# Kernel optimization log

Measured on AMD Instinct MI355X. Metric: run time of the kernel, lower is better.

The kernel has to match this reference:

```python
import jax, jax.numpy as jnp
import numpy as np

L, B, T, I, H, O = 2, 64, 256, 512, 1024, 256
HIDDEN_WEIGHT = 0.5  # placement_weight = 1 - hidden_weight
# dropout is identity in eval mode (reference is deterministic)


def setup_inputs() -> dict:
    key = jax.random.key(0)
    ks = jax.random.split(key, 20)
    def unif(k, shape, fan):
        b = 1.0 / np.sqrt(fan)
        return jax.random.uniform(k, shape, jnp.float32, -b, b)
    lengths = jax.random.randint(ks[4], (B,), 0, T + 1)
    lengths = lengths.at[0].set(T).at[1].set(0)  # exercise full-length and zero-length paths
    return {
        "step_input": jax.random.normal(ks[0], (B, T, I), jnp.float32),
        "clstm_hidden": jax.random.normal(ks[1], (B, H), jnp.float32),
        "hidden": jax.random.normal(ks[2], (L, B, H), jnp.float32),
        "cell": jax.random.normal(ks[3], (L, B, H), jnp.float32),
        "input_lengths": lengths.astype(jnp.int64),
        # LSTM params, PyTorch gate order [i, f, g, o]
        "w_ih0": unif(ks[5], (4 * H, I), H), "w_hh0": unif(ks[6], (4 * H, H), H),
        "b_ih0": unif(ks[7], (4 * H,), H), "b_hh0": unif(ks[8], (4 * H,), H),
        "w_ih1": unif(ks[9], (4 * H, H), H), "w_hh1": unif(ks[10], (4 * H, H), H),
        "b_ih1": unif(ks[11], (4 * H,), H), "b_hh1": unif(ks[12], (4 * H,), H),
        "w1": unif(ks[13], (H, H), H), "b1": unif(ks[14], (H,), H),
        "w2": unif(ks[15], (O, H), H), "b2": unif(ks[16], (O,), H),
    }


def compute_weighted_hidden(clstm_hidden, hidden, lens):
    # vectorized version of the per-(layer,batch) min-max rescale loop
    cmin = jnp.min(clstm_hidden, axis=-1, keepdims=True)            # [B,1]
    crange = jnp.max(clstm_hidden, axis=-1, keepdims=True) - cmin   # [B,1]
    safe_cr = jnp.where(crange > 0, crange, 1.0)
    s = jnp.where(crange > 0, (clstm_hidden - cmin) / safe_cr, clstm_hidden)  # [B,H]
    hmin = jnp.min(hidden, axis=-1, keepdims=True)                  # [L,B,1]
    hrange = jnp.max(hidden, axis=-1, keepdims=True) - hmin         # [L,B,1]
    s2 = jnp.where(hrange > 0, hmin + s[None] * hrange,
                   jnp.broadcast_to(s[None], hidden.shape))         # [L,B,H]
    c = jnp.where((lens == 0)[None, :, None], clstm_hidden[None], s2)
    return HIDDEN_WEIGHT * hidden + (1.0 - HIDDEN_WEIGHT) * c


def lstm_forward(x, h0, c0, lens, layer_params):
    # x: [B,T,I]; h0,c0: [L,B,H]; lens already clamped to >=1
    t_idx = jnp.arange(x.shape[1])

    def step(carry, xt_t):
        h, c = carry                      # each [L,B,H]
        xt, t = xt_t                      # xt: [B,I]
        valid = (t < lens)[:, None]       # [B,1]
        inp = xt
        hs, cs = [], []
        for l, (wih, whh, bih, bhh) in enumerate(layer_params):
            gates = inp @ wih.T + bih + h[l] @ whh.T + bhh   # [B,4H]
            i, f, g, o = jnp.split(gates, 4, axis=-1)
            i, f, o = jax.nn.sigmoid(i), jax.nn.sigmoid(f), jax.nn.sigmoid(o)
            g = jnp.tanh(g)
            c_new = f * c[l] + i * g
            h_new = o * jnp.tanh(c_new)
            hs.append(jnp.where(valid, h_new, h[l]))
            cs.append(jnp.where(valid, c_new, c[l]))
            inp = jnp.where(valid, h_new, 0.0)
        out_t = inp                        # top layer output, zeroed on padding
        return (jnp.stack(hs), jnp.stack(cs)), out_t

    (hn, cn), outs = jax.lax.scan(step, (h0, c0), (x.transpose(1, 0, 2), t_idx))
    return outs.transpose(1, 0, 2), hn, cn  # [B,T,H], [L,B,H], [L,B,H]


def reference(step_input, clstm_hidden, hidden, cell, input_lengths,
              w_ih0, w_hh0, b_ih0, b_hh0, w_ih1, w_hh1, b_ih1, b_hh1,
              w1, b1, w2, b2):
    weighted_hidden = compute_weighted_hidden(clstm_hidden, hidden, input_lengths)
    lens = jnp.clip(input_lengths, 1, None)  # torch.clamp(min=1)
    layer_params = [(w_ih0, w_hh0, b_ih0, b_hh0), (w_ih1, w_hh1, b_ih1, b_hh1)]
    lstm_out, hn, cn = lstm_forward(step_input, weighted_hidden, cell, lens, layer_params)
    # dropout layers are identity in eval mode
    h1 = jax.nn.relu(lstm_out @ w1.T + b1)
    logits = jax.nn.relu(h1 @ w2.T + b2)  # [B,T,O]
    zero = (input_lengths == 0)
    logits = jnp.where(zero[:, None, None], 0.0, logits)
    hn = jnp.where(zero[None, :, None], 0.0, hn)
    cn = jnp.where(zero[None, :, None], 0.0, cn)
    return logits, hn, cn
```

## Files before the change

### kernel.cpp

```cpp
#include <hip/hip_runtime.h>


typedef __bf16 bf16x8 __attribute__((ext_vector_type(8)));
typedef float f32x4 __attribute__((ext_vector_type(4)));
typedef int i32x4 __attribute__((ext_vector_type(4)));

__device__ __forceinline__ unsigned short f2bf(float f) {
  unsigned u = __float_as_uint(f);
  u = u + 0x7FFFu + ((u >> 16) & 1u);
  return (unsigned short)(u >> 16);
}
__device__ __forceinline__ float sigm_(float x) { return 1.f / (1.f + __expf(-x)); }
__device__ __forceinline__ float tanh_(float x) { return 1.f - 2.f / (__expf(2.f * x) + 1.f); }

__device__ __forceinline__ int hxoff(int b, int u) {
  return (b >> 4) * 16384 + (u >> 5) * 512 + ((u >> 3) & 3) * 128 + (b & 15) * 8 + (u & 7);
}

__global__ void cvt_kernel(const float* __restrict__ s, unsigned short* __restrict__ d, int n) {
  int i = (blockIdx.x * 256 + threadIdx.x) * 4;
  if (i < n) {
    float4 v = *reinterpret_cast<const float4*>(s + i);
    ushort4 o = make_ushort4(f2bf(v.x), f2bf(v.y), f2bf(v.z), f2bf(v.w));
    *reinterpret_cast<ushort4*>(d + i) = o;
  }
}

__global__ __launch_bounds__(256) void prep_kernel(
    const float* __restrict__ clstm, const float* __restrict__ hidden,
    const float* __restrict__ cell, const int* __restrict__ lens,
    float* __restrict__ hstate, float* __restrict__ cstate,
    unsigned short* __restrict__ h0buf, unsigned short* __restrict__ h1buf,
    const float* __restrict__ bih0, const float* __restrict__ bhh0,
    const float* __restrict__ bih1, const float* __restrict__ bhh1,
    float* __restrict__ bias0, float* __restrict__ bias1p,
    unsigned* __restrict__ bar) {
  const int tid = threadIdx.x, blk = blockIdx.x;
  const int l = blk >> 6, b = blk & 63;
  const float* crow = clstm + b * 1024;
  const float* hrow = hidden + ((size_t)l * 64 + b) * 1024;
  float cmn = 3.4e38f, cmx = -3.4e38f, hmn = 3.4e38f, hmx = -3.4e38f;
  for (int i = tid; i < 1024; i += 256) {
    float c = crow[i], h = hrow[i];
    cmn = fminf(cmn, c); cmx = fmaxf(cmx, c);
    hmn = fminf(hmn, h); hmx = fmaxf(hmx, h);
  }
#pragma unroll
  for (int off = 32; off > 0; off >>= 1) {
    cmn = fminf(cmn, __shfl_xor(cmn, off));
    cmx = fmaxf(cmx, __shfl_xor(cmx, off));
    hmn = fminf(hmn, __shfl_xor(hmn, off));
    hmx = fmaxf(hmx, __shfl_xor(hmx, off));
  }
  __shared__ float red[4][4];
  int wv = tid >> 6;
  if ((tid & 63) == 0) { red[wv][0] = cmn; red[wv][1] = cmx; red[wv][2] = hmn; red[wv][3] = hmx; }
  __syncthreads();
  cmn = fminf(fminf(red[0][0], red[1][0]), fminf(red[2][0], red[3][0]));
  cmx = fmaxf(fmaxf(red[0][1], red[1][1]), fmaxf(red[2][1], red[3][1]));
  hmn = fminf(fminf(red[0][2], red[1][2]), fminf(red[2][2], red[3][2]));
  hmx = fmaxf(fmaxf(red[0][3], red[1][3]), fmaxf(red[2][3], red[3][3]));
  const float crange = cmx - cmn, hrange = hmx - hmn;
  const int len = lens[b];
  const size_t base = ((size_t)l * 64 + b) * 1024;
  unsigned short* dst = (l == 0) ? h0buf : (h1buf + 65536);
  for (int i = tid; i < 1024; i += 256) {
    float cv = crow[i], hv = hrow[i];
    float s = (crange > 0.f) ? (cv - cmn) / crange : cv;
    float s2 = (hrange > 0.f) ? (hmn + s * hrange) : s;
    float cc = (len == 0) ? cv : s2;
    float w = 0.5f * hv + 0.5f * cc;
    hstate[base + i] = w;
    cstate[base + i] = cell[base + i];
    dst[hxoff(b, i)] = f2bf(w);
  }
  if (blk == 0) {
    for (int n = tid; n < 4096; n += 256) {
      bias0[n] = bih0[n] + bhh0[n];
      bias1p[(n & 1023) * 4 + (n >> 10)] = bih1[n] + bhh1[n];
    }
    for (int n = tid; n < 32768; n += 256) bar[n] = 0u;
  }
}

template <int AMODE, int EPI>
__global__ __launch_bounds__(256) void gemm_kernel(
    const void* __restrict__ Ap, const unsigned short* __restrict__ Bw,
    void* __restrict__ Cout, const float* __restrict__ bias,
    const int* __restrict__ lens, int M, int N, int K, int t0) {
  __shared__ unsigned short Al[128][40];
  __shared__ unsigned short Bl[128][40];
  const int tid = threadIdx.x;
  const int m0 = blockIdx.y * 128, n0 = blockIdx.x * 128;
  const int srow = tid >> 2;
  const int c8 = (tid & 3) * 8;
  size_t aoff0, aoff1;
  {
    int r = m0 + srow, r2 = r + 64;
    if (AMODE == 0) {
      aoff0 = (size_t)r * K; aoff1 = (size_t)r2 * K;
    } else {
      aoff0 = ((size_t)(r & 63) * 256 + t0 + (r >> 6)) * K;
      aoff1 = ((size_t)(r2 & 63) * 256 + t0 + (r2 >> 6)) * K;
    }
  }
  const size_t boff0 = (size_t)(n0 + srow) * K, boff1 = (size_t)(n0 + srow + 64) * K;
  const int wave = tid >> 6, lane = tid & 63, ln = lane & 15, quad = lane >> 4;
  const int mq = (wave >> 1) * 64, nq = (wave & 1) * 64;
  f32x4 acc[4][4] = {};
  const int nkt = K >> 5;
  for (int kt = 0; kt < nkt; ++kt) {
    const int kc = kt * 32 + c8;
    if (AMODE == 1) {
      const float* A = (const float*)Ap;
      const float* p0 = A + aoff0 + kc;
      const float* p1 = A + aoff1 + kc;
      float4 v0 = *reinterpret_cast<const float4*>(p0);
      float4 v0b = *reinterpret_cast<const float4*>(p0 + 4);
      float4 v1 = *reinterpret_cast<const float4*>(p1);
      float4 v1b = *reinterpret_cast<const float4*>(p1 + 4);
      *reinterpret_cast<ushort4*>(&Al[srow][c8]) =
          make_ushort4(f2bf(v0.x), f2bf(v0.y), f2bf(v0.z), f2bf(v0.w));
      *reinterpret_cast<ushort4*>(&Al[srow][c8 + 4]) =
          make_ushort4(f2bf(v0b.x), f2bf(v0b.y), f2bf(v0b.z), f2bf(v0b.w));
      *reinterpret_cast<ushort4*>(&Al[srow + 64][c8]) =
          make_ushort4(f2bf(v1.x), f2bf(v1.y), f2bf(v1.z), f2bf(v1.w));
      *reinterpret_cast<ushort4*>(&Al[srow + 64][c8 + 4]) =
          make_ushort4(f2bf(v1b.x), f2bf(v1b.y), f2bf(v1b.z), f2bf(v1b.w));
    } else {
      const unsigned short* A = (const unsigned short*)Ap;
      *reinterpret_cast<int4*>(&Al[srow][c8]) = *reinterpret_cast<const int4*>(A + aoff0 + kc);
      *reinterpret_cast<int4*>(&Al[srow + 64][c8]) = *reinterpret_cast<const int4*>(A + aoff1 + kc);
    }
    *reinterpret_cast<int4*>(&Bl[srow][c8]) = *reinterpret_cast<const int4*>(Bw + boff0 + kc);
    *reinterpret_cast<int4*>(&Bl[srow + 64][c8]) = *reinterpret_cast<const int4*>(Bw + boff1 + kc);
    __syncthreads();
    bf16x8 af[4], bfr[4];
#pragma unroll
    for (int i = 0; i < 4; ++i) {
      af[i] = *reinterpret_cast<const bf16x8*>(&Al[mq + i * 16 + ln][quad * 8]);
      bfr[i] = *reinterpret_cast<const bf16x8*>(&Bl[nq + i * 16 + ln][quad * 8]);
    }
#pragma unroll
    for (int i = 0; i < 4; ++i)
#pragma unroll
      for (int j = 0; j < 4; ++j)
        acc[i][j] = __builtin_amdgcn_mfma_f32_16x16x32_bf16(af[i], bfr[j], acc[i][j], 0, 0, 0);
    __syncthreads();
  }
#pragma unroll
  for (int i = 0; i < 4; ++i) {
    int mmb = m0 + mq + i * 16 + quad * 4;
#pragma unroll
    for (int j = 0; j < 4; ++j) {
      int nn = n0 + nq + j * 16 + ln;
      float bv = bias[nn];
#pragma unroll
      for (int r = 0; r < 4; ++r) {
        int mm = mmb + r;
        float v = acc[i][j][r] + bv;
        if (EPI >= 1) v = fmaxf(v, 0.f);
        if (EPI == 2) {
          if (lens[mm >> 8] == 0) v = 0.f;
          ((float*)Cout)[(size_t)mm * N + nn] = v;
        } else if (EPI == 1) {
          ((unsigned short*)Cout)[(size_t)mm * N + nn] = f2bf(v);
        } else {
          size_t idx = ((size_t)mm * 128 + ((nn >> 3) & 127)) * 32 + (nn & 7) * 4 + (nn >> 10);
          ((float*)Cout)[idx] = v;
        }
      }
    }
  }
}

#define HLo(dst, ptr, off) \
  asm volatile("global_load_dwordx4 %0, %1, off offset:" off " sc0 sc1" \
               : "=v"(dst) : "v"(ptr))
#define HL4(h0, h1, h2, h3, ptr) \
  HLo(h0, ptr, "0"); HLo(h1, ptr, "1024"); HLo(h2, ptr, "2048"); HLo(h3, ptr, "3072")
#define HLF(dst, ptr) \
  asm volatile("global_load_dwordx4 %0, %1, off sc0 sc1" : "=v"(dst) : "v"(ptr))
#define HST(ptr, val) \
  asm volatile("global_store_dwordx4 %0, %1, off sc0 sc1" :: "v"(ptr), "v"(val) : "memory")

__global__ __launch_bounds__(512) void rec2_kernel(
    const unsigned short* __restrict__ whh0b,
    const unsigned short* __restrict__ wih1b,
    const unsigned short* __restrict__ whh1b,
    const float* __restrict__ G2,
    const float* __restrict__ bias1p,
    unsigned short* __restrict__ h0buf,
    unsigned short* __restrict__ h1buf,
    float* __restrict__ pre1buf,
    float* __restrict__ hstate, float* __restrict__ cstate,
    unsigned short* __restrict__ h1out,
    const int* __restrict__ lens, int t0, int nint, unsigned* __restrict__ bar) {
  __shared__ unsigned short wlds[32 * 1032];
  __shared__ float glds[2][64][73];
  __shared__ unsigned short hsh[64][16];
  const int tid = threadIdx.x;
  const int bid = blockIdx.x;
  const bool isL1 = bid >= 128;
  const int g = bid & 127;
  {
    int r = tid >> 4;
    int c0 = (tid & 15) * 64;
    const unsigned short* src;
    if (!isL1)
      src = wih1b + (size_t)((r >> 3) * 1024 + g * 8 + (r & 7)) * 1024;
    else
      src = whh1b + (size_t)((2 + (r >> 4)) * 1024 + g * 16 + (r & 15)) * 1024;
    const i32x4* s4 = reinterpret_cast<const i32x4*>(src + c0);
    i32x4* dst = reinterpret_cast<i32x4*>(wlds + r * 1032 + c0);
#pragma unroll
    for (int j = 0; j < 8; ++j) dst[j] = s4[j];
  }
  const int wave = tid >> 6, lane = tid & 63, ln = lane & 15, quad = lane >> 4;
  const int mt = wave & 3, kw = wave >> 2;
  bf16x8 bregA[16], bregB[16];
  {
    const unsigned short *bpA, *bpB;
    if (!isL1) {
      bpA = whh0b + (size_t)((ln >> 3) * 1024 + g * 8 + (ln & 7)) * 1024 + kw * 512 + quad * 8;
      bpB = whh0b + (size_t)((2 + (ln >> 3)) * 1024 + g * 8 + (ln & 7)) * 1024 + kw * 512 + quad * 8;
    } else {
      bpA = whh1b + (size_t)(g * 16 + ln) * 1024 + kw * 512 + quad * 8;
      bpB = whh1b + (size_t)(1024 + g * 16 + ln) * 1024 + kw * 512 + quad * 8;
    }
#pragma unroll
    for (int kt = 0; kt < 16; ++kt) {
      bregA[kt] = *reinterpret_cast<const bf16x8*>(bpA + kt * 32);
      bregB[kt] = *reinterpret_cast<const bf16x8*>(bpB + kt * 32);
    }
  }
  const int b = tid >> 3, ul = tid & 7;
  const size_t sb0 = (size_t)(isL1 ? 65536 : 0) + (size_t)b * 1024 +
                     (isL1 ? g * 16 + ul : g * 8 + ul);
  float cm0 = cstate[sb0], hm0 = hstate[sb0];
  float cm1 = 0.f, hm1 = 0.f;
  if (isL1) { cm1 = cstate[sb0 + 8]; hm1 = hstate[sb0 + 8]; }
  int lv0 = lens[b];
  const int len = lv0 < 1 ? 1 : lv0;
  int lvA = lens[mt * 16 + ln];
  const int lenmA = lvA < 1 ? 1 : lvA;
  f32x4 b1a = {0.f, 0.f, 0.f, 0.f}, b1b = {0.f, 0.f, 0.f, 0.f};
  if (isL1) {
    b1a = *reinterpret_cast<const f32x4*>(bias1p + (g * 16 + ul) * 4);
    b1b = *reinterpret_cast<const f32x4*>(bias1p + (g * 16 + 8 + ul) * 4);
  }
  int lenp = 257;
  if (isL1 && tid < 128) { int lv = lens[tid >> 1]; lenp = lv < 1 ? 1 : lv; }
  const int puboff = (tid >> 4) * 16384 + (g >> 2) * 512 + (g & 3) * 128 + (tid & 15) * 8;
  const int pub1off = ((tid >> 1) >> 4) * 16384 + (g >> 1) * 512 +
                      ((g * 2 + (tid & 1)) & 3) * 128 + ((tid >> 1) & 15) * 8;
  const bf16x8 z8 = {};
  const i32x4 zi = {};
  __syncthreads();

  for (int k = 0; k < nint; ++k) {
    const int s = t0 + k;
    const bool actG = (!isL1) && (k < 64);
    const bool actP = (!isL1) && (s >= 1) && (s <= 256);
    const bool actL = isL1 && (s >= 2);
    if (actG || actP || actL) {
      f32x4 pga = {0.f, 0.f, 0.f, 0.f}, pgb = {0.f, 0.f, 0.f, 0.f};
      if (isL1) {
        const float* pr = pre1buf + (size_t)((s - 2) & 3) * 262144 +
                          ((size_t)b * 1024 + g * 16) * 4;
        HLF(pga, pr + ul * 4);
        HLF(pgb, pr + (8 + ul) * 4);
      }
      bf16x8 hf[16];
      const unsigned short* p = (isL1 ? h1buf + ((s - 1) & 1) * 65536
                                      : h0buf + (s & 1) * 65536) +
                                mt * 16384 + kw * 8192 + lane * 8;
      HL4(hf[0], hf[1], hf[2], hf[3], p);
      HL4(hf[4], hf[5], hf[6], hf[7], p + 2048);
      HL4(hf[8], hf[9], hf[10], hf[11], p + 4096);
      HL4(hf[12], hf[13], hf[14], hf[15], p + 6144);
      if (actG)
        pga = *reinterpret_cast<const f32x4*>(
            G2 + (((size_t)(k * 64 + b)) * 128 + g) * 32 + ul * 4);
      const bool maskA = (!isL1) && ((s - 1) >= lenmA);
      f32x4 acc0 = {0.f, 0.f, 0.f, 0.f}, acc1 = acc0, acc2 = acc0, acc3 = acc0;
      const unsigned short* wp = wlds + ln * 1032 + kw * 512 + quad * 8;
      asm volatile("s_waitcnt vmcnt(8)" ::: "memory");
      __builtin_amdgcn_sched_barrier(0);
#pragma unroll
      for (int kt = 0; kt < 8; ++kt) {
        const unsigned short* c = wp + kt * 32;
        bf16x8 bC = *reinterpret_cast<const bf16x8*>(c);
        bf16x8 bD = *reinterpret_cast<const bf16x8*>(c + 16512);
        bf16x8 a_ = hf[kt];
        acc0 = __builtin_amdgcn_mfma_f32_16x16x32_bf16(a_, bregA[kt], acc0, 0, 0, 0);
        acc1 = __builtin_amdgcn_mfma_f32_16x16x32_bf16(a_, bregB[kt], acc1, 0, 0, 0);
        bf16x8 am = maskA ? z8 : a_;
        acc2 = __builtin_amdgcn_mfma_f32_16x16x32_bf16(am, bC, acc2, 0, 0, 0);
        acc3 = __builtin_amdgcn_mfma_f32_16x16x32_bf16(am, bD, acc3, 0, 0, 0);
      }
      asm volatile("s_waitcnt vmcnt(0)" ::: "memory");
      __builtin_amdgcn_sched_barrier(0);
#pragma unroll
      for (int kt = 8; kt < 16; ++kt) {
        const unsigned short* c = wp + kt * 32;
        bf16x8 bC = *reinterpret_cast<const bf16x8*>(c);
        bf16x8 bD = *reinterpret_cast<const bf16x8*>(c + 16512);
        bf16x8 a_ = hf[kt];
        acc0 = __builtin_amdgcn_mfma_f32_16x16x32_bf16(a_, bregA[kt], acc0, 0, 0, 0);
        acc1 = __builtin_amdgcn_mfma_f32_16x16x32_bf16(a_, bregB[kt], acc1, 0, 0, 0);
        bf16x8 am = maskA ? z8 : a_;
        acc2 = __builtin_amdgcn_mfma_f32_16x16x32_bf16(am, bC, acc2, 0, 0, 0);
        acc3 = __builtin_amdgcn_mfma_f32_16x16x32_bf16(am, bD, acc3, 0, 0, 0);
      }
#pragma unroll
      for (int r = 0; r < 4; ++r) {
        float* gp = &glds[kw][mt * 16 + quad * 4 + r][0];
        gp[ln] = acc0[r]; gp[16 + ln] = acc1[r];
        gp[32 + ln] = acc2[r]; gp[48 + ln] = acc3[r];
      }
      __syncthreads();
      const float* g0 = &glds[0][b][0];
      const float* g1 = &glds[1][b][0];
      if (actG) {
        float pi = g0[ul] + g1[ul] + pga.x;
        float pf = g0[8 + ul] + g1[8 + ul] + pga.y;
        float pgg = g0[16 + ul] + g1[16 + ul] + pga.z;
        float po = g0[24 + ul] + g1[24 + ul] + pga.w;
        float ig = sigm_(pi), fg = sigm_(pf), gv = tanh_(pgg), og = sigm_(po);
        float cn_ = fg * cm0 + ig * gv;
        float hn_ = og * tanh_(cn_);
        if (s < len) { cm0 = cn_; hm0 = hn_; }
        hsh[b][ul] = f2bf(hm0);
      }
      if (actP) {
        f32x4 pv;
        pv.x = g0[32 + ul] + g1[32 + ul];
        pv.y = g0[40 + ul] + g1[40 + ul];
        pv.z = g0[48 + ul] + g1[48 + ul];
        pv.w = g0[56 + ul] + g1[56 + ul];
        float* pd = pre1buf + (size_t)((s - 1) & 3) * 262144 +
                    (size_t)b * 4096 + g * 32 + ul * 4;
        HST(pd, pv);
      }
      if (actL) {
        {
          float pi = g0[ul] + g1[ul] + pga.x + b1a.x;
          float pf = g0[16 + ul] + g1[16 + ul] + pga.y + b1a.y;
          float pgg = g0[32 + ul] + g1[32 + ul] + pga.z + b1a.z;
          float po = g0[48 + ul] + g1[48 + ul] + pga.w + b1a.w;
          float ig = sigm_(pi), fg = sigm_(pf), gv = tanh_(pgg), og = sigm_(po);
          float cn_ = fg * cm0 + ig * gv;
          float hn_ = og * tanh_(cn_);
          if (s - 2 < len) { cm0 = cn_; hm0 = hn_; }
          hsh[b][ul] = f2bf(hm0);
        }
        {
          int iu = 8 + ul;
          float pi = g0[iu] + g1[iu] + pgb.x + b1b.x;
          float pf = g0[16 + iu] + g1[16 + iu] + pgb.y + b1b.y;
          float pgg = g0[32 + iu] + g1[32 + iu] + pgb.z + b1b.z;
          float po = g0[48 + iu] + g1[48 + iu] + pgb.w + b1b.w;
          float ig = sigm_(pi), fg = sigm_(pf), gv = tanh_(pgg), og = sigm_(po);
          float cn_ = fg * cm1 + ig * gv;
          float hn_ = og * tanh_(cn_);
          if (s - 2 < len) { cm1 = cn_; hm1 = hn_; }
          hsh[b][iu] = f2bf(hm1);
        }
      }
      __syncthreads();
      if (!isL1) {
        if (actG && tid < 64) {
          i32x4 v = *reinterpret_cast<const i32x4*>(&hsh[tid][0]);
          unsigned short* d = h0buf + ((s + 1) & 1) * 65536 + puboff;
          HST(d, v);
        }
        asm volatile("s_waitcnt vmcnt(0)" ::: "memory");
      } else {
        if (tid < 128) {
          const int pb = tid >> 1, half = tid & 1;
          i32x4 v = *reinterpret_cast<const i32x4*>(&hsh[pb][half * 8]);
          unsigned short* d = h1buf + (s & 1) * 65536 + pub1off;
          HST(d, v);
          const int t = s - 2;
          i32x4 vo = (t < lenp) ? v : zi;
          *reinterpret_cast<i32x4*>(h1out + ((size_t)pb * 256 + t) * 1024 +
                                    g * 16 + half * 8) = vo;
          asm volatile("s_waitcnt vmcnt(1)" ::: "memory");
        }
      }
    }
    __syncthreads();
    if (tid == 0) {
      const unsigned val = (unsigned)(s + 1);
#pragma unroll
      for (int rep = 0; rep < 8; ++rep)
        __hip_atomic_store(bar + ((bid * 8 + rep) << 4), val,
                           __ATOMIC_RELAXED, __HIP_MEMORY_SCOPE_AGENT);
    }
    const bool lastk = (k == nint - 1) && (nint == 66);
    if (tid < 192 && !lastk) {
      const int tgt = (tid < 128) ? (s + 1) : (isL1 ? (s + 1) : (s - 1));
      if (tgt > 0) {
        const unsigned* lp = bar + ((tid * 8 + (bid & 7)) << 4);
        while ((int)__hip_atomic_load(lp, __ATOMIC_RELAXED,
                                      __HIP_MEMORY_SCOPE_AGENT) < tgt)
          __builtin_amdgcn_s_sleep(2);
      }
    }
    __syncthreads();
  }
  hstate[sb0] = hm0; cstate[sb0] = cm0;
  if (isL1) { hstate[sb0 + 8] = hm1; cstate[sb0 + 8] = cm1; }
}

__global__ void final_kernel(const float* __restrict__ hstate, const float* __restrict__ cstate,
                             const int* __restrict__ lens, float* __restrict__ out) {
  int i = blockIdx.x * 256 + threadIdx.x;
  int b = (i >> 10) & 63;
  float z = (lens[b] == 0) ? 0.f : 1.f;
  out[4194304 + i] = z * hstate[i];
  out[4325376 + i] = z * cstate[i];
}

extern "C" void kernel_launch(void* const* d_in, const int* in_sizes, int n_in,
                              void* d_out, int out_size, void* d_ws, size_t ws_size,
                              hipStream_t stream) {
  const float* x = (const float*)d_in[0];
  const float* clstm = (const float*)d_in[1];
  const float* hidden = (const float*)d_in[2];
  const float* cell = (const float*)d_in[3];
  const int* lens = (const int*)d_in[4];
  const float* wih0 = (const float*)d_in[5];
  const float* whh0 = (const float*)d_in[6];
  const float* bih0 = (const float*)d_in[7];
  const float* bhh0 = (const float*)d_in[8];
  const float* wih1 = (const float*)d_in[9];
  const float* whh1 = (const float*)d_in[10];
  const float* bih1 = (const float*)d_in[11];
  const float* bhh1 = (const float*)d_in[12];
  const float* w1 = (const float*)d_in[13];
  const float* b1 = (const float*)d_in[14];
  const float* w2 = (const float*)d_in[15];
  const float* b2 = (const float*)d_in[16];
  float* out = (float*)d_out;

  char* ws = (char*)d_ws;
  size_t off = 0;
  auto alloc = [&](size_t bytes) -> void* {
    void* p = ws + off;
    off += (bytes + 255) & ~(size_t)255;
    return p;
  };
  unsigned short* wih0_b = (unsigned short*)alloc(2097152ull * 2);
  unsigned short* whh0_b = (unsigned short*)alloc(4194304ull * 2);
  unsigned short* wih1_b = (unsigned short*)alloc(4194304ull * 2);
  unsigned short* whh1_b = (unsigned short*)alloc(4194304ull * 2);
  unsigned short* w1_b = (unsigned short*)alloc(1048576ull * 2);
  unsigned short* w2_b = (unsigned short*)alloc(262144ull * 2);
  float* bias0 = (float*)alloc(4096 * 4);
  float* bias1p = (float*)alloc(4096 * 4);
  float* hstate = (float*)alloc(131072ull * 4);
  float* cstate = (float*)alloc(131072ull * 4);
  unsigned short* h0buf = (unsigned short*)alloc(131072ull * 2);
  unsigned short* h1buf = (unsigned short*)alloc(131072ull * 2);
  float* pre1buf = (float*)alloc(1048576ull * 4);
  unsigned* bar = (unsigned*)alloc(131072);
  float* G = (float*)alloc(16777216ull * 4);
  unsigned short* h1out = (unsigned short*)alloc(16777216ull * 2);

  cvt_kernel<<<2048, 256, 0, stream>>>(wih0, wih0_b, 2097152);
  cvt_kernel<<<4096, 256, 0, stream>>>(whh0, whh0_b, 4194304);
  cvt_kernel<<<4096, 256, 0, stream>>>(wih1, wih1_b, 4194304);
  cvt_kernel<<<4096, 256, 0, stream>>>(whh1, whh1_b, 4194304);
  cvt_kernel<<<1024, 256, 0, stream>>>(w1, w1_b, 1048576);
  cvt_kernel<<<256, 256, 0, stream>>>(w2, w2_b, 262144);

  prep_kernel<<<128, 256, 0, stream>>>(clstm, hidden, cell, lens, hstate, cstate,
                                       h0buf, h1buf, bih0, bhh0, bih1, bhh1,
                                       bias0, bias1p, bar);

  for (int c = 0; c < 4; ++c) {
    gemm_kernel<1, 0><<<dim3(32, 32), 256, 0, stream>>>(x, wih0_b, G, bias0, lens,
                                                        4096, 4096, 512, c * 64);
    rec2_kernel<<<192, 512, 0, stream>>>(whh0_b, wih1_b, whh1_b, G, bias1p,
                                         h0buf, h1buf, pre1buf, hstate, cstate,
                                         h1out, lens, c * 64, (c == 3) ? 66 : 64, bar);
  }
  gemm_kernel<0, 1><<<dim3(8, 128), 256, 0, stream>>>(h1out, w1_b, (void*)G, b1, lens,
                                                      16384, 1024, 1024, 0);
  gemm_kernel<0, 2><<<dim3(2, 128), 256, 0, stream>>>((const void*)G, w2_b, out, b2, lens,
                                                      16384, 256, 1024, 0);
  final_kernel<<<512, 256, 0, stream>>>(hstate, cstate, lens, out);
}
```

Measured before the change: 2.062 ms.

## Replace block-wide barriers with per-wave-pair flags and per-row-tile grid barriers

Each workgroup's four batch row tiles (mt) now synchronise independently. Pairs of waves handshake through LDS flags instead of __syncthreads. The cross-block grid barrier is split per row tile, so each tile only waits on producers of the same tile and can run ahead of the others. A staggered startup sleep spreads the tiles out in time, and the barrier array is enlarged, with its zeroing spread across all prep blocks. This is meant to cut whole-block and whole-grid stalls in the latency-bound recurrence, at the cost of more flag traffic and tricky memory ordering.

Result: slower. 2.955 ms (+43.3%).

```diff
diff --git a/kernel.cpp b/kernel.cpp
--- a/kernel.cpp
+++ b/kernel.cpp
@@ -74,12 +74,12 @@
     cstate[base + i] = cell[base + i];
     dst[hxoff(b, i)] = f2bf(w);
   }
+  for (int n = tid; n < 1024; n += 256) bar[blk * 1024 + n] = 0u;
   if (blk == 0) {
     for (int n = tid; n < 4096; n += 256) {
       bias0[n] = bih0[n] + bhh0[n];
       bias1p[(n & 1023) * 4 + (n >> 10)] = bih1[n] + bhh1[n];
     }
-    for (int n = tid; n < 32768; n += 256) bar[n] = 0u;
   }
 }
 
@@ -176,13 +176,22 @@
 
 #define HLo(dst, ptr, off) \
   asm volatile("global_load_dwordx4 %0, %1, off offset:" off " sc0 sc1" \
-               : "=v"(dst) : "v"(ptr))
+               : "=v"(dst) : "v"(ptr) : "memory")
 #define HL4(h0, h1, h2, h3, ptr) \
   HLo(h0, ptr, "0"); HLo(h1, ptr, "1024"); HLo(h2, ptr, "2048"); HLo(h3, ptr, "3072")
 #define HLF(dst, ptr) \
-  asm volatile("global_load_dwordx4 %0, %1, off sc0 sc1" : "=v"(dst) : "v"(ptr))
+  asm volatile("global_load_dwordx4 %0, %1, off sc0 sc1" : "=v"(dst) : "v"(ptr) : "memory")
 #define HST(ptr, val) \
   asm volatile("global_store_dwordx4 %0, %1, off sc0 sc1" :: "v"(ptr), "v"(val) : "memory")
+
+#define PSYNC(ph, ep) do { \
+    if (lane == 0) \
+      __hip_atomic_store(&flg[mt][kw][ph], (unsigned)(ep), __ATOMIC_RELEASE, \
+                         __HIP_MEMORY_SCOPE_WORKGROUP); \
+    while (__hip_atomic_load(&flg[mt][kw ^ 1][ph], __ATOMIC_ACQUIRE, \
+                             __HIP_MEMORY_SCOPE_WORKGROUP) < (unsigned)(ep)) \
+      __builtin_amdgcn_s_sleep(1); \
+  } while (0)
 
 __global__ __launch_bounds__(512) void rec2_kernel(
     const unsigned short* __restrict__ whh0b,
@@ -199,10 +208,12 @@
   __shared__ unsigned short wlds[32 * 1032];
   __shared__ float glds[2][64][73];
   __shared__ unsigned short hsh[64][16];
+  __shared__ unsigned flg[4][2][4];
   const int tid = threadIdx.x;
   const int bid = blockIdx.x;
   const bool isL1 = bid >= 128;
   const int g = bid & 127;
+  if (tid < 32) ((unsigned*)flg)[tid] = 0;
   {
     int r = tid >> 4;
     int c0 = (tid & 15) * 64;
@@ -218,6 +229,7 @@
   }
   const int wave = tid >> 6, lane = tid & 63, ln = lane & 15, quad = lane >> 4;
   const int mt = wave & 3, kw = wave >> 2;
+  const int p = (kw << 6) | lane;
   bf16x8 bregA[16], bregB[16];
   {
     const unsigned short *bpA, *bpB;
@@ -234,7 +246,7 @@
       bregB[kt] = *reinterpret_cast<const bf16x8*>(bpB + kt * 32);
     }
   }
-  const int b = tid >> 3, ul = tid & 7;
+  const int b = mt * 16 + (p >> 3), ul = p & 7;
   const size_t sb0 = (size_t)(isL1 ? 65536 : 0) + (size_t)b * 1024 +
                      (isL1 ? g * 16 + ul : g * 8 + ul);
   float cm0 = cstate[sb0], hm0 = hstate[sb0];
@@ -250,16 +262,19 @@
     b1b = *reinterpret_cast<const f32x4*>(bias1p + (g * 16 + 8 + ul) * 4);
   }
   int lenp = 257;
-  if (isL1 && tid < 128) { int lv = lens[tid >> 1]; lenp = lv < 1 ? 1 : lv; }
-  const int puboff = (tid >> 4) * 16384 + (g >> 2) * 512 + (g & 3) * 128 + (tid & 15) * 8;
-  const int pub1off = ((tid >> 1) >> 4) * 16384 + (g >> 1) * 512 +
-                      ((g * 2 + (tid & 1)) & 3) * 128 + ((tid >> 1) & 15) * 8;
+  if (isL1 && p < 32) { int lv = lens[mt * 16 + (p >> 1)]; lenp = lv < 1 ? 1 : lv; }
+  const int puboff = mt * 16384 + (g >> 2) * 512 + (g & 3) * 128 + (p & 15) * 8;
+  const int pub1off = mt * 16384 + (g >> 1) * 512 + ((g * 2 + (p & 1)) & 3) * 128 +
+                      ((p >> 1) & 15) * 8;
   const bf16x8 z8 = {};
   const i32x4 zi = {};
   __syncthreads();
 
   for (int k = 0; k < nint; ++k) {
     const int s = t0 + k;
+    if (k == 0 && mt) {
+      for (int i = 0; i < mt * 6; ++i) __builtin_amdgcn_s_sleep(7);
+    }
     const bool actG = (!isL1) && (k < 64);
     const bool actP = (!isL1) && (s >= 1) && (s <= 256);
     const bool actL = isL1 && (s >= 2);
@@ -272,13 +287,13 @@
         HLF(pgb, pr + (8 + ul) * 4);
       }
       bf16x8 hf[16];
-      const unsigned short* p = (isL1 ? h1buf + ((s - 1) & 1) * 65536
-                                      : h0buf + (s & 1) * 65536) +
-                                mt * 16384 + kw * 8192 + lane * 8;
-      HL4(hf[0], hf[1], hf[2], hf[3], p);
-      HL4(hf[4], hf[5], hf[6], hf[7], p + 2048);
-      HL4(hf[8], hf[9], hf[10], hf[11], p + 4096);
-      HL4(hf[12], hf[13], hf[14], hf[15], p + 6144);
+      const unsigned short* pp = (isL1 ? h1buf + ((s - 1) & 1) * 65536
+                                       : h0buf + (s & 1) * 65536) +
+                                 mt * 16384 + kw * 8192 + lane * 8;
+      HL4(hf[0], hf[1], hf[2], hf[3], pp);
+      HL4(hf[4], hf[5], hf[6], hf[7], pp + 2048);
+      HL4(hf[8], hf[9], hf[10], hf[11], pp + 4096);
+      HL4(hf[12], hf[13], hf[14], hf[15], pp + 6144);
       if (actG)
         pga = *reinterpret_cast<const f32x4*>(
             G2 + (((size_t)(k * 64 + b)) * 128 + g) * 32 + ul * 4);
@@ -319,7 +334,7 @@
         gp[ln] = acc0[r]; gp[16 + ln] = acc1[r];
         gp[32 + ln] = acc2[r]; gp[48 + ln] = acc3[r];
       }
-      __syncthreads();
+      PSYNC(0, k + 1);
       const float* g0 = &glds[0][b][0];
       const float* g1 = &glds[1][b][0];
       if (actG) {
@@ -368,17 +383,18 @@
           hsh[b][iu] = f2bf(hm1);
         }
       }
-      __syncthreads();
+      if (kw) { asm volatile("s_waitcnt vmcnt(0)" ::: "memory"); }
+      PSYNC(1, k + 1);
       if (!isL1) {
-        if (actG && tid < 64) {
-          i32x4 v = *reinterpret_cast<const i32x4*>(&hsh[tid][0]);
+        if (actG && p < 16) {
+          i32x4 v = *reinterpret_cast<const i32x4*>(&hsh[mt * 16 + p][0]);
           unsigned short* d = h0buf + ((s + 1) & 1) * 65536 + puboff;
           HST(d, v);
         }
         asm volatile("s_waitcnt vmcnt(0)" ::: "memory");
       } else {
-        if (tid < 128) {
-          const int pb = tid >> 1, half = tid & 1;
+        if (p < 32) {
+          const int pb = mt * 16 + (p >> 1), half = p & 1;
           i32x4 v = *reinterpret_cast<const i32x4*>(&hsh[pb][half * 8]);
           unsigned short* d = h1buf + (s & 1) * 65536 + pub1off;
           HST(d, v);
@@ -386,29 +402,37 @@
           i32x4 vo = (t < lenp) ? v : zi;
           *reinterpret_cast<i32x4*>(h1out + ((size_t)pb * 256 + t) * 1024 +
                                     g * 16 + half * 8) = vo;
-          asm volatile("s_waitcnt vmcnt(1)" ::: "memory");
         }
-      }
-    }
-    __syncthreads();
-    if (tid == 0) {
+        asm volatile("s_waitcnt vmcnt(1)" ::: "memory");
+      }
+    }
+    if (p == 0) {
       const unsigned val = (unsigned)(s + 1);
+      const int sidx = (bid * 4 + mt) * 8;
 #pragma unroll
       for (int rep = 0; rep < 8; ++rep)
-        __hip_atomic_store(bar + ((bid * 8 + rep) << 4), val,
+        __hip_atomic_store(bar + ((sidx + rep) << 4), val,
                            __ATOMIC_RELAXED, __HIP_MEMORY_SCOPE_AGENT);
     }
     const bool lastk = (k == nint - 1) && (nint == 66);
-    if (tid < 192 && !lastk) {
-      const int tgt = (tid < 128) ? (s + 1) : (isL1 ? (s + 1) : (s - 1));
-      if (tgt > 0) {
-        const unsigned* lp = bar + ((tid * 8 + (bid & 7)) << 4);
+    if (!lastk) {
+      {
+        const unsigned* lp = bar + (((p * 4 + mt) * 8 + (bid & 7)) << 4);
         while ((int)__hip_atomic_load(lp, __ATOMIC_RELAXED,
-                                      __HIP_MEMORY_SCOPE_AGENT) < tgt)
+                                      __HIP_MEMORY_SCOPE_AGENT) < s + 1)
           __builtin_amdgcn_s_sleep(2);
       }
-    }
-    __syncthreads();
+      if (p < 64) {
+        const int tgt = isL1 ? (s + 1) : (s - 1);
+        if (tgt > 0) {
+          const unsigned* lp = bar + ((((128 + p) * 4 + mt) * 8 + (bid & 7)) << 4);
+          while ((int)__hip_atomic_load(lp, __ATOMIC_RELAXED,
+                                        __HIP_MEMORY_SCOPE_AGENT) < tgt)
+            __builtin_amdgcn_s_sleep(2);
+        }
+      }
+      PSYNC(2, k + 1);
+    }
   }
   hstate[sb0] = hm0; cstate[sb0] = cm0;
   if (isL1) { hstate[sb0 + 8] = hm1; cstate[sb0 + 8] = cm1; }
@@ -465,7 +489,7 @@
   unsigned short* h0buf = (unsigned short*)alloc(131072ull * 2);
   unsigned short* h1buf = (unsigned short*)alloc(131072ull * 2);
   float* pre1buf = (float*)alloc(1048576ull * 4);
-  unsigned* bar = (unsigned*)alloc(131072);
+  unsigned* bar = (unsigned*)alloc(524288);
   float* G = (float*)alloc(16777216ull * 4);
   unsigned short* h1out = (unsigned short*)alloc(16777216ull * 2);
 
```
